# Performance work log

Hardware: AMD Instinct MI355X
Metric: run time of the kernel (lower is better)

Reference implementation:

```python
import jax, jax.numpy as jnp
import numpy as np

VOCAB, H, MAXLEN = 50257, 1024, 128


def setup_inputs() -> dict:
    key = jax.random.key(0)
    ks = jax.random.split(key, 14)
    s = 0.02  # init scale
    f32 = jnp.float32
    return {
        "x": jax.random.randint(ks[0], (1,), 0, VOCAB),
        "h": jax.random.normal(ks[1], (1, 1, H), f32),
        "encoder_outputs": jax.random.normal(ks[2], (MAXLEN, H), f32),
        "emb": jax.random.normal(ks[3], (VOCAB, H), f32) * s,
        "W_attn": jax.random.normal(ks[4], (MAXLEN, 2 * H), f32) * s,
        "b_attn": jnp.zeros((MAXLEN,), f32),
        "W_comb": jax.random.normal(ks[5], (H, 2 * H), f32) * s,
        "b_comb": jnp.zeros((H,), f32),
        "w_ih": jax.random.normal(ks[6], (3 * H, H), f32) * s,
        "w_hh": jax.random.normal(ks[7], (3 * H, H), f32) * s,
        "b_ih": jnp.zeros((3 * H,), f32),
        "b_hh": jnp.zeros((3 * H,), f32),
        "W_out": jax.random.normal(ks[8], (VOCAB, H), f32) * s,
        "b_out": jnp.zeros((VOCAB,), f32),
    }


def reference(x, h, encoder_outputs, emb, W_attn, b_attn, W_comb, b_comb,
              w_ih, w_hh, b_ih, b_hh, W_out, b_out):
    # Single decode step (batch=1, seq=1); dropout in eval mode (identity).
    e = emb[x]                       # [1, H] embedded token
    h0 = h[0]                        # [1, H] hidden state
    # attention over encoder outputs
    attn_w = jax.nn.softmax(jnp.concatenate([e, h0], axis=1) @ W_attn.T + b_attn, axis=1)  # [1, MAXLEN]
    attn_applied = attn_w @ encoder_outputs                                                 # [1, H]
    # combine + relu
    g = jax.nn.relu(jnp.concatenate([e, attn_applied], axis=1) @ W_comb.T + b_comb)        # [1, H]
    # single-step GRU (PyTorch gate order: r, z, n)
    gi = g @ w_ih.T + b_ih           # [1, 3H]
    gh = h0 @ w_hh.T + b_hh          # [1, 3H]
    i_r, i_z, i_n = jnp.split(gi, 3, axis=1)
    h_r, h_z, h_n = jnp.split(gh, 3, axis=1)
    r = jax.nn.sigmoid(i_r + h_r)
    z = jax.nn.sigmoid(i_z + h_z)
    n = jnp.tanh(i_n + r * h_n)
    h_new = (1.0 - z) * n + z * h0   # [1, H]
    out = jax.nn.log_softmax(h_new @ W_out.T + b_out, axis=1)  # [1, VOCAB]
    return out, h_new[None], attn_w
```

## Files before the change

kernel.cpp:

```cpp
#include <hip/hip_runtime.h>
#include <hip/hip_bf16.h>
#include <math.h>

#define H 1024
#define MAXLEN 128
#define VOCAB 50257
#define NB_OUT ((VOCAB + 3) / 4)

__device__ inline float wave_reduce_sum(float v) {
    #pragma unroll
    for (int off = 32; off > 0; off >>= 1) v += __shfl_down(v, off);
    return v;
}

__global__ void k_attn_logits(const int* x, const float* h, const float* emb,
                              const float* W_attn, const float* b_attn, float* logits) {
    const int row = blockIdx.x;
    const float4* w4 = (const float4*)(W_attn + row * (2 * H));
    const float4* e4 = (const float4*)(emb + (long long)x[0] * H);
    const float4* h4 = (const float4*)h;
    float acc = 0.f;
    int t = threadIdx.x;
    #pragma unroll
    for (int i = 0; i < 2; i++) {
        int idx = t + i * 256;
        float4 wv = w4[idx];
        float4 cv = (idx < 256) ? e4[idx] : h4[idx - 256];
        acc += wv.x * cv.x + wv.y * cv.y + wv.z * cv.z + wv.w * cv.w;
    }
    __shared__ float red[4];
    int lane = t & 63, wid = t >> 6;
    acc = wave_reduce_sum(acc);
    if (lane == 0) red[wid] = acc;
    __syncthreads();
    if (t == 0)
        logits[row] = red[0] + red[1] + red[2] + red[3] + b_attn[row];
}

__global__ void k_attn_sm_apply(const float* logits, const float* enc,
                                float* attn_applied, float* out_attn) {
    __shared__ float buf[MAXLEN];
    __shared__ float w[MAXLEN];
    int t = threadIdx.x;
    if (t < MAXLEN) buf[t] = logits[t];
    __syncthreads();
    float m = -INFINITY;
    #pragma unroll 8
    for (int k = 0; k < MAXLEN; k++) m = fmaxf(m, buf[k]);
    if (t < MAXLEN) w[t] = expf(buf[t] - m);
    __syncthreads();
    float s = 0.f;
    #pragma unroll 8
    for (int k = 0; k < MAXLEN; k++) s += w[k];
    float inv = 1.f / s;
    int j = blockIdx.x * blockDim.x + t;
    float acc = 0.f;
    #pragma unroll 8
    for (int k = 0; k < MAXLEN; k++) acc += w[k] * enc[k * H + j];
    attn_applied[j] = acc * inv;
    if (blockIdx.x == 0 && t < MAXLEN) out_attn[t] = w[t] * inv;
}

__global__ void k_combine(const int* x, const float* emb, const float* attn_applied,
                          const float* W_comb, const float* b_comb, float* g) {
    int wid = threadIdx.x >> 6, lane = threadIdx.x & 63;
    int row = blockIdx.x * 4 + wid;
    const float4* w4 = (const float4*)(W_comb + (long long)row * (2 * H));
    const float4* e4 = (const float4*)(emb + (long long)x[0] * H);
    const float4* a4 = (const float4*)attn_applied;
    float acc = 0.f;
    #pragma unroll
    for (int i = 0; i < 8; i++) {
        int idx = lane + i * 64;
        float4 wv = w4[idx];
        float4 cv = (idx < 256) ? e4[idx] : a4[idx - 256];
        acc += wv.x * cv.x + wv.y * cv.y + wv.z * cv.z + wv.w * cv.w;
    }
    acc = wave_reduce_sum(acc);
    if (lane == 0) g[row] = fmaxf(acc + b_comb[row], 0.f);
}

__global__ void k_gru_mm(const float* g, const float* h,
                         const float* w_ih, const float* w_hh,
                         const float* b_ih, const float* b_hh,
                         float* gi, float* gh) {
    int wid = threadIdx.x >> 6, lane = threadIdx.x & 63;
    int gRow = blockIdx.x * 4 + wid;
    const float* vec;
    const float* mat;
    const float* bias;
    float* out;
    int row;
    if (gRow < 3 * H) { row = gRow; vec = g; mat = w_ih; bias = b_ih; out = gi; }
    else { row = gRow - 3 * H; vec = h; mat = w_hh; bias = b_hh; out = gh; }
    const float4* w4 = (const float4*)(mat + (long long)row * H);
    const float4* v4 = (const float4*)vec;
    float acc = 0.f;
    #pragma unroll
    for (int i = 0; i < 4; i++) {
        int idx = lane + i * 64;
        float4 wv = w4[idx];
        float4 vv = v4[idx];
        acc += wv.x * vv.x + wv.y * vv.y + wv.z * vv.z + wv.w * vv.w;
    }
    acc = wave_reduce_sum(acc);
    if (lane == 0) out[row] = acc + bias[row];
}

__global__ void k_gates(const float* gi, const float* gh, const float* h, float* h_new) {
    int j = threadIdx.x;
    float r = 1.f / (1.f + expf(-(gi[j] + gh[j])));
    float z = 1.f / (1.f + expf(-(gi[j + H] + gh[j + H])));
    float n = tanhf(gi[j + 2 * H] + r * gh[j + 2 * H]);
    h_new[j] = (1.f - z) * n + z * h[j];
}

__global__ void k_out_matvec(const float* hn, const float* W_out, const float* b_out,
                             float* out, float* pmax, float* psum) {
    int wid = threadIdx.x >> 6, lane = threadIdx.x & 63;
    int row = blockIdx.x * 4 + wid;
    __shared__ float lm[4];
    float logit = -INFINITY;
    if (row < VOCAB) {
        const float4* w4 = (const float4*)(W_out + (long long)row * H);
        const float4* h4 = (const float4*)hn;
        float acc = 0.f;
        #pragma unroll
        for (int i = 0; i < 4; i++) {
            int idx = lane + i * 64;
            float4 wv = w4[idx];
            float4 hv = h4[idx];
            acc += wv.x * hv.x + wv.y * hv.y + wv.z * hv.z + wv.w * hv.w;
        }
        acc = wave_reduce_sum(acc);
        if (lane == 0) { logit = acc + b_out[row]; out[row] = logit; }
    }
    if (lane == 0) lm[wid] = logit;
    __syncthreads();
    if (threadIdx.x == 0) {
        float m = fmaxf(fmaxf(lm[0], lm[1]), fmaxf(lm[2], lm[3]));
        float s = 0.f;
        #pragma unroll
        for (int i = 0; i < 4; i++)
            if (lm[i] != -INFINITY) s += expf(lm[i] - m);
        pmax[blockIdx.x] = m;
        psum[blockIdx.x] = s;
    }
}

__global__ void k_lse_merge(const float* pmax, const float* psum, float* c) {
    __shared__ float red[16];
    __shared__ float Msh;
    int lane = threadIdx.x & 63, wid = threadIdx.x >> 6;
    float m = -INFINITY;
    for (int i = threadIdx.x; i < NB_OUT; i += blockDim.x) m = fmaxf(m, pmax[i]);
    #pragma unroll
    for (int off = 32; off > 0; off >>= 1) m = fmaxf(m, __shfl_down(m, off));
    if (lane == 0) red[wid] = m;
    __syncthreads();
    if (threadIdx.x == 0) {
        float mm = red[0];
        for (int i = 1; i < 16; i++) mm = fmaxf(mm, red[i]);
        Msh = mm;
    }
    __syncthreads();
    float M = Msh;
    float s = 0.f;
    for (int i = threadIdx.x; i < NB_OUT; i += blockDim.x) s += psum[i] * expf(pmax[i] - M);
    s = wave_reduce_sum(s);
    if (lane == 0) red[wid] = s;
    __syncthreads();
    if (threadIdx.x == 0) {
        float ss = 0.f;
        for (int i = 0; i < 16; i++) ss += red[i];
        c[0] = M + logf(ss);
    }
}

__global__ void k_sub(float* out, const float* c) {
    int v = blockIdx.x * blockDim.x + threadIdx.x;
    if (v < VOCAB) out[v] -= c[0];
}

extern "C" void kernel_launch(void* const* d_in, const int* in_sizes, int n_in,
                              void* d_out, int out_size, void* d_ws, size_t ws_size,
                              hipStream_t stream) {
    const int*   x     = (const int*)d_in[0];
    const float* h     = (const float*)d_in[1];
    const float* enc   = (const float*)d_in[2];
    const float* emb   = (const float*)d_in[3];
    const float* W_attn= (const float*)d_in[4];
    const float* b_attn= (const float*)d_in[5];
    const float* W_comb= (const float*)d_in[6];
    const float* b_comb= (const float*)d_in[7];
    const float* w_ih  = (const float*)d_in[8];
    const float* w_hh  = (const float*)d_in[9];
    const float* b_ih  = (const float*)d_in[10];
    const float* b_hh  = (const float*)d_in[11];
    const float* W_out = (const float*)d_in[12];
    const float* b_out = (const float*)d_in[13];

    float* out      = (float*)d_out;
    float* out_h    = out + VOCAB;
    float* out_attn = out + VOCAB + H;

    float* ws       = (float*)d_ws;
    float* logits128   = ws;
    float* attn_applied= ws + 256;
    float* g           = ws + 1280;
    float* gi          = ws + 2304;
    float* gh          = ws + 5376;
    float* lse_c       = ws + 8448;
    float* pmax        = ws + 9216;
    float* psum        = ws + 22272;

    k_attn_logits<<<MAXLEN, 256, 0, stream>>>(x, h, emb, W_attn, b_attn, logits128);
    k_attn_sm_apply<<<H / 256, 256, 0, stream>>>(logits128, enc, attn_applied, out_attn);
    k_combine<<<H / 4, 256, 0, stream>>>(x, emb, attn_applied, W_comb, b_comb, g);
    k_gru_mm<<<(6 * H) / 4, 256, 0, stream>>>(g, h, w_ih, w_hh, b_ih, b_hh, gi, gh);
    k_gates<<<1, H, 0, stream>>>(gi, gh, h, out_h);
    k_out_matvec<<<NB_OUT, 256, 0, stream>>>(out_h, W_out, b_out, out, pmax, psum);
    k_lse_merge<<<1, 1024, 0, stream>>>(pmax, psum, lse_c);
    k_sub<<<(VOCAB + 255) / 256, 256, 0, stream>>>(out, lse_c);
}
```

Before: 74.12 us.

## Fuse decoder prefix into persistent kernel with grid barriers; fold LSE merge into projection

The attention, combine, GRU matvecs and gates stages are merged into one 256-block kernel that separates stages with software grid barriers on atomic counters. Gate computation is fused with the GRU matvecs so each wave computes all six rows for one hidden unit. The output projection uses 1024-thread blocks and has the last block, chosen by an atomic ticket, perform the log-sum-exp merge. This cuts the number of kernel launches from eight to three, plus a memset. The risk is that the grid barrier deadlocks if the 256 blocks are not all resident at once, and it adds spin-wait overhead.

```diff
diff --git a/kernel.cpp b/kernel.cpp
--- a/kernel.cpp
+++ b/kernel.cpp
@@ -1,11 +1,15 @@
 #include <hip/hip_runtime.h>
-#include <hip/hip_bf16.h>
 #include <math.h>
 
 #define H 1024
 #define MAXLEN 128
 #define VOCAB 50257
-#define NB_OUT ((VOCAB + 3) / 4)
+
+#define NB_A 256
+#define NT_A 256
+#define NT_B 1024
+#define ROWS_B 16
+#define NB_B ((VOCAB + ROWS_B - 1) / ROWS_B)
 
 __device__ inline float wave_reduce_sum(float v) {
     #pragma unroll
@@ -13,167 +17,205 @@
     return v;
 }
 
-__global__ void k_attn_logits(const int* x, const float* h, const float* emb,
-                              const float* W_attn, const float* b_attn, float* logits) {
-    const int row = blockIdx.x;
-    const float4* w4 = (const float4*)(W_attn + row * (2 * H));
+__device__ inline float dot4(float4 a, float4 b) {
+    return a.x * b.x + a.y * b.y + a.z * b.z + a.w * b.w;
+}
+
+__device__ inline void sw_barrier(unsigned* ctr, unsigned nb) {
+    __syncthreads();
+    if (threadIdx.x == 0) {
+        __threadfence();
+        __hip_atomic_fetch_add(ctr, 1u, __ATOMIC_ACQ_REL, __HIP_MEMORY_SCOPE_AGENT);
+        while (__hip_atomic_load(ctr, __ATOMIC_ACQUIRE, __HIP_MEMORY_SCOPE_AGENT) < nb) {
+            __builtin_amdgcn_s_sleep(1);
+        }
+        __threadfence();
+    }
+    __syncthreads();
+}
+
+__global__ void __launch_bounds__(NT_A, 4) k_prefix(
+    const int* x, const float* h, const float* enc, const float* emb,
+    const float* W_attn, const float* b_attn,
+    const float* W_comb, const float* b_comb,
+    const float* w_ih, const float* w_hh, const float* b_ih, const float* b_hh,
+    float* out_h, float* out_attn,
+    float* logits128, float* attn_applied, float* g_vec,
+    unsigned* bar)
+{
+    const int bid = blockIdx.x, t = threadIdx.x;
+    const int lane = t & 63, wid = t >> 6;
+    const int gw = bid * 4 + wid;
     const float4* e4 = (const float4*)(emb + (long long)x[0] * H);
     const float4* h4 = (const float4*)h;
-    float acc = 0.f;
-    int t = threadIdx.x;
+
+    if (gw < MAXLEN) {
+        const float4* w4 = (const float4*)(W_attn + gw * (2 * H));
+        float acc = 0.f;
+        #pragma unroll
+        for (int i = 0; i < 8; i++) {
+            int idx = lane + i * 64;
+            float4 wv = w4[idx];
+            float4 cv = (idx < 256) ? e4[idx] : h4[idx - 256];
+            acc += dot4(wv, cv);
+        }
+        acc = wave_reduce_sum(acc);
+        if (lane == 0) logits128[gw] = acc + b_attn[gw];
+    }
+    sw_barrier(&bar[0], NB_A);
+
+    if (bid < H / NT_A) {
+        __shared__ float buf[MAXLEN];
+        __shared__ float wsm[MAXLEN];
+        if (t < MAXLEN) buf[t] = logits128[t];
+        __syncthreads();
+        float m = -INFINITY;
+        #pragma unroll 8
+        for (int k = 0; k < MAXLEN; k++) m = fmaxf(m, buf[k]);
+        if (t < MAXLEN) wsm[t] = expf(buf[t] - m);
+        __syncthreads();
+        float s = 0.f;
+        #pragma unroll 8
+        for (int k = 0; k < MAXLEN; k++) s += wsm[k];
+        float inv = 1.f / s;
+        int j = bid * NT_A + t;
+        float acc = 0.f;
+        #pragma unroll 8
+        for (int k = 0; k < MAXLEN; k++) acc += wsm[k] * enc[k * H + j];
+        attn_applied[j] = acc * inv;
+        if (bid == 0 && t < MAXLEN) out_attn[t] = wsm[t] * inv;
+    }
+    sw_barrier(&bar[1], NB_A);
+
+    {
+        int row = gw;
+        const float4* w4 = (const float4*)(W_comb + (long long)row * (2 * H));
+        const float4* a4 = (const float4*)attn_applied;
+        float acc = 0.f;
+        #pragma unroll
+        for (int i = 0; i < 8; i++) {
+            int idx = lane + i * 64;
+            float4 wv = w4[idx];
+            float4 cv = (idx < 256) ? e4[idx] : a4[idx - 256];
+            acc += dot4(wv, cv);
+        }
+        acc = wave_reduce_sum(acc);
+        if (lane == 0) g_vec[row] = fmaxf(acc + b_comb[row], 0.f);
+    }
+    sw_barrier(&bar[2], NB_A);
+
+    {
+        int j = gw;
+        const float4* g4 = (const float4*)g_vec;
+        float4 vg[4], vh[4];
+        #pragma unroll
+        for (int i = 0; i < 4; i++) {
+            int idx = lane + i * 64;
+            vg[i] = g4[idx];
+            vh[i] = h4[idx];
+        }
+        float a6[6];
+        #pragma unroll
+        for (int gt = 0; gt < 3; gt++) {
+            const float4* wi = (const float4*)(w_ih + (long long)(j + gt * H) * H);
+            const float4* wh = (const float4*)(w_hh + (long long)(j + gt * H) * H);
+            float ai = 0.f, ah = 0.f;
+            #pragma unroll
+            for (int i = 0; i < 4; i++) {
+                int idx = lane + i * 64;
+                ai += dot4(wi[idx], vg[i]);
+                ah += dot4(wh[idx], vh[i]);
+            }
+            a6[gt] = ai;
+            a6[3 + gt] = ah;
+        }
+        #pragma unroll
+        for (int k = 0; k < 6; k++) a6[k] = wave_reduce_sum(a6[k]);
+        if (lane == 0) {
+            float gi_r = a6[0] + b_ih[j];
+            float gi_z = a6[1] + b_ih[j + H];
+            float gi_n = a6[2] + b_ih[j + 2 * H];
+            float gh_r = a6[3] + b_hh[j];
+            float gh_z = a6[4] + b_hh[j + H];
+            float gh_n = a6[5] + b_hh[j + 2 * H];
+            float r = 1.f / (1.f + expf(-(gi_r + gh_r)));
+            float z = 1.f / (1.f + expf(-(gi_z + gh_z)));
+            float n = tanhf(gi_n + r * gh_n);
+            out_h[j] = (1.f - z) * n + z * h[j];
+        }
+    }
+}
+
+__global__ void __launch_bounds__(NT_B, 2) k_project(
+    const float* hn, const float* W_out, const float* b_out,
+    float* out, float* pmax, float* psum, float* lse_c, unsigned* ticket)
+{
+    const int t = threadIdx.x;
+    const int lane = t & 63, wid = t >> 6;
+    const int row = blockIdx.x * ROWS_B + wid;
+    __shared__ float lm[ROWS_B];
+    __shared__ int islast;
+
+    const float4* h4 = (const float4*)hn;
+    float4 hreg[4];
     #pragma unroll
-    for (int i = 0; i < 2; i++) {
-        int idx = t + i * 256;
-        float4 wv = w4[idx];
-        float4 cv = (idx < 256) ? e4[idx] : h4[idx - 256];
-        acc += wv.x * cv.x + wv.y * cv.y + wv.z * cv.z + wv.w * cv.w;
-    }
-    __shared__ float red[4];
-    int lane = t & 63, wid = t >> 6;
-    acc = wave_reduce_sum(acc);
-    if (lane == 0) red[wid] = acc;
-    __syncthreads();
-    if (t == 0)
-        logits[row] = red[0] + red[1] + red[2] + red[3] + b_attn[row];
-}
-
-__global__ void k_attn_sm_apply(const float* logits, const float* enc,
-                                float* attn_applied, float* out_attn) {
-    __shared__ float buf[MAXLEN];
-    __shared__ float w[MAXLEN];
-    int t = threadIdx.x;
-    if (t < MAXLEN) buf[t] = logits[t];
-    __syncthreads();
-    float m = -INFINITY;
-    #pragma unroll 8
-    for (int k = 0; k < MAXLEN; k++) m = fmaxf(m, buf[k]);
-    if (t < MAXLEN) w[t] = expf(buf[t] - m);
-    __syncthreads();
-    float s = 0.f;
-    #pragma unroll 8
-    for (int k = 0; k < MAXLEN; k++) s += w[k];
-    float inv = 1.f / s;
-    int j = blockIdx.x * blockDim.x + t;
-    float acc = 0.f;
-    #pragma unroll 8
-    for (int k = 0; k < MAXLEN; k++) acc += w[k] * enc[k * H + j];
-    attn_applied[j] = acc * inv;
-    if (blockIdx.x == 0 && t < MAXLEN) out_attn[t] = w[t] * inv;
-}
-
-__global__ void k_combine(const int* x, const float* emb, const float* attn_applied,
-                          const float* W_comb, const float* b_comb, float* g) {
-    int wid = threadIdx.x >> 6, lane = threadIdx.x & 63;
-    int row = blockIdx.x * 4 + wid;
-    const float4* w4 = (const float4*)(W_comb + (long long)row * (2 * H));
-    const float4* e4 = (const float4*)(emb + (long long)x[0] * H);
-    const float4* a4 = (const float4*)attn_applied;
-    float acc = 0.f;
-    #pragma unroll
-    for (int i = 0; i < 8; i++) {
-        int idx = lane + i * 64;
-        float4 wv = w4[idx];
-        float4 cv = (idx < 256) ? e4[idx] : a4[idx - 256];
-        acc += wv.x * cv.x + wv.y * cv.y + wv.z * cv.z + wv.w * cv.w;
-    }
-    acc = wave_reduce_sum(acc);
-    if (lane == 0) g[row] = fmaxf(acc + b_comb[row], 0.f);
-}
-
-__global__ void k_gru_mm(const float* g, const float* h,
-                         const float* w_ih, const float* w_hh,
-                         const float* b_ih, const float* b_hh,
-                         float* gi, float* gh) {
-    int wid = threadIdx.x >> 6, lane = threadIdx.x & 63;
-    int gRow = blockIdx.x * 4 + wid;
-    const float* vec;
-    const float* mat;
-    const float* bias;
-    float* out;
-    int row;
-    if (gRow < 3 * H) { row = gRow; vec = g; mat = w_ih; bias = b_ih; out = gi; }
-    else { row = gRow - 3 * H; vec = h; mat = w_hh; bias = b_hh; out = gh; }
-    const float4* w4 = (const float4*)(mat + (long long)row * H);
-    const float4* v4 = (const float4*)vec;
-    float acc = 0.f;
-    #pragma unroll
-    for (int i = 0; i < 4; i++) {
-        int idx = lane + i * 64;
-        float4 wv = w4[idx];
-        float4 vv = v4[idx];
-        acc += wv.x * vv.x + wv.y * vv.y + wv.z * vv.z + wv.w * vv.w;
-    }
-    acc = wave_reduce_sum(acc);
-    if (lane == 0) out[row] = acc + bias[row];
-}
-
-__global__ void k_gates(const float* gi, const float* gh, const float* h, float* h_new) {
-    int j = threadIdx.x;
-    float r = 1.f / (1.f + expf(-(gi[j] + gh[j])));
-    float z = 1.f / (1.f + expf(-(gi[j + H] + gh[j + H])));
-    float n = tanhf(gi[j + 2 * H] + r * gh[j + 2 * H]);
-    h_new[j] = (1.f - z) * n + z * h[j];
-}
-
-__global__ void k_out_matvec(const float* hn, const float* W_out, const float* b_out,
-                             float* out, float* pmax, float* psum) {
-    int wid = threadIdx.x >> 6, lane = threadIdx.x & 63;
-    int row = blockIdx.x * 4 + wid;
-    __shared__ float lm[4];
+    for (int i = 0; i < 4; i++) hreg[i] = h4[lane + i * 64];
+
     float logit = -INFINITY;
     if (row < VOCAB) {
         const float4* w4 = (const float4*)(W_out + (long long)row * H);
-        const float4* h4 = (const float4*)hn;
-        float acc = 0.f;
-        #pragma unroll
-        for (int i = 0; i < 4; i++) {
-            int idx = lane + i * 64;
-            float4 wv = w4[idx];
-            float4 hv = h4[idx];
-            acc += wv.x * hv.x + wv.y * hv.y + wv.z * hv.z + wv.w * hv.w;
-        }
+        float acc = 0.f;
+        #pragma unroll
+        for (int i = 0; i < 4; i++) acc += dot4(w4[lane + i * 64], hreg[i]);
         acc = wave_reduce_sum(acc);
         if (lane == 0) { logit = acc + b_out[row]; out[row] = logit; }
     }
     if (lane == 0) lm[wid] = logit;
     __syncthreads();
-    if (threadIdx.x == 0) {
-        float m = fmaxf(fmaxf(lm[0], lm[1]), fmaxf(lm[2], lm[3]));
+    if (t == 0) {
+        float m = -INFINITY;
+        #pragma unroll
+        for (int i = 0; i < ROWS_B; i++) m = fmaxf(m, lm[i]);
         float s = 0.f;
         #pragma unroll
-        for (int i = 0; i < 4; i++)
+        for (int i = 0; i < ROWS_B; i++)
             if (lm[i] != -INFINITY) s += expf(lm[i] - m);
         pmax[blockIdx.x] = m;
         psum[blockIdx.x] = s;
-    }
-}
-
-__global__ void k_lse_merge(const float* pmax, const float* psum, float* c) {
-    __shared__ float red[16];
-    __shared__ float Msh;
-    int lane = threadIdx.x & 63, wid = threadIdx.x >> 6;
-    float m = -INFINITY;
-    for (int i = threadIdx.x; i < NB_OUT; i += blockDim.x) m = fmaxf(m, pmax[i]);
-    #pragma unroll
-    for (int off = 32; off > 0; off >>= 1) m = fmaxf(m, __shfl_down(m, off));
-    if (lane == 0) red[wid] = m;
-    __syncthreads();
-    if (threadIdx.x == 0) {
-        float mm = red[0];
-        for (int i = 1; i < 16; i++) mm = fmaxf(mm, red[i]);
-        Msh = mm;
-    }
-    __syncthreads();
-    float M = Msh;
-    float s = 0.f;
-    for (int i = threadIdx.x; i < NB_OUT; i += blockDim.x) s += psum[i] * expf(pmax[i] - M);
-    s = wave_reduce_sum(s);
-    if (lane == 0) red[wid] = s;
-    __syncthreads();
-    if (threadIdx.x == 0) {
-        float ss = 0.f;
-        for (int i = 0; i < 16; i++) ss += red[i];
-        c[0] = M + logf(ss);
+        __threadfence();
+        unsigned old = __hip_atomic_fetch_add(ticket, 1u, __ATOMIC_ACQ_REL, __HIP_MEMORY_SCOPE_AGENT);
+        islast = (old == (unsigned)(gridDim.x - 1)) ? 1 : 0;
+    }
+    __syncthreads();
+    if (islast) {
+        __threadfence();
+        __shared__ float red[ROWS_B];
+        float m = -INFINITY;
+        for (int i = t; i < NB_B; i += NT_B) m = fmaxf(m, pmax[i]);
+        #pragma unroll
+        for (int off = 32; off > 0; off >>= 1) m = fmaxf(m, __shfl_down(m, off));
+        if (lane == 0) red[wid] = m;
+        __syncthreads();
+        if (t == 0) {
+            float mm = red[0];
+            #pragma unroll
+            for (int i = 1; i < ROWS_B; i++) mm = fmaxf(mm, red[i]);
+            red[0] = mm;
+        }
+        __syncthreads();
+        float M = red[0];
+        float s = 0.f;
+        for (int i = t; i < NB_B; i += NT_B) s += psum[i] * expf(pmax[i] - M);
+        s = wave_reduce_sum(s);
+        __syncthreads();
+        if (lane == 0) red[wid] = s;
+        __syncthreads();
+        if (t == 0) {
+            float ss = 0.f;
+            #pragma unroll
+            for (int i = 0; i < ROWS_B; i++) ss += red[i];
+            lse_c[0] = M + logf(ss);
+        }
     }
 }
 
@@ -204,22 +246,22 @@
     float* out_h    = out + VOCAB;
     float* out_attn = out + VOCAB + H;
 
-    float* ws       = (float*)d_ws;
+    float* ws          = (float*)d_ws;
     float* logits128   = ws;
     float* attn_applied= ws + 256;
-    float* g           = ws + 1280;
-    float* gi          = ws + 2304;
-    float* gh          = ws + 5376;
-    float* lse_c       = ws + 8448;
-    float* pmax        = ws + 9216;
-    float* psum        = ws + 22272;
-
-    k_attn_logits<<<MAXLEN, 256, 0, stream>>>(x, h, emb, W_attn, b_attn, logits128);
-    k_attn_sm_apply<<<H / 256, 256, 0, stream>>>(logits128, enc, attn_applied, out_attn);
-    k_combine<<<H / 4, 256, 0, stream>>>(x, emb, attn_applied, W_comb, b_comb, g);
-    k_gru_mm<<<(6 * H) / 4, 256, 0, stream>>>(g, h, w_ih, w_hh, b_ih, b_hh, gi, gh);
-    k_gates<<<1, H, 0, stream>>>(gi, gh, h, out_h);
-    k_out_matvec<<<NB_OUT, 256, 0, stream>>>(out_h, W_out, b_out, out, pmax, psum);
-    k_lse_merge<<<1, 1024, 0, stream>>>(pmax, psum, lse_c);
-    k_sub<<<(VOCAB + 255) / 256, 256, 0, stream>>>(out, lse_c);
-}
+    float* g_vec       = ws + 1280;
+    float* lse_c       = ws + 2304;
+    float* pmax        = ws + 4096;
+    float* psum        = ws + 8192;
+    unsigned* bar      = (unsigned*)((char*)d_ws + 65536);
+
+    hipMemsetAsync((void*)bar, 0, 16, stream);
+
+    k_prefix<<<NB_A, NT_A, 0, stream>>>(x, h, enc, emb, W_attn, b_attn,
+                                        W_comb, b_comb, w_ih, w_hh, b_ih, b_hh,
+                                        out_h, out_attn,
+                                        logits128, attn_applied, g_vec, bar);
+    k_project<<<NB_B, NT_B, 0, stream>>>(out_h, W_out, b_out,
+                                         out, pmax, psum, lse_c, &bar[3]);
+    k_sub<<<(VOCAB + 1023) / 1024, 1024, 0, stream>>>(out, lse_c);
+}
```

Result: slower. 283.2 us (+282.1%).
